# Kernel tuning notes

Hardware: AMD Instinct MI355X
Metric: run time of the kernel (lower is better)

The kernel has to match this reference:

```python
import jax, jax.numpy as jnp
import numpy as np

B, L, H, NH, HD, IT = 16, 512, 256, 8, 32, 2
NEG = -9e15


def _ln(x, g, b):
    m = x.mean(-1, keepdims=True)
    v = ((x - m) ** 2).mean(-1, keepdims=True)
    return (x - m) / jnp.sqrt(v + 1e-5) * g + b


def setup_inputs() -> dict:
    key = jax.random.key(0)
    ks = jax.random.split(key, 12)

    def nrm(k, shape, fan_in):
        return jax.random.normal(k, shape, dtype=jnp.float32) / np.float32(np.sqrt(fan_in))

    return {
        "data": jax.random.normal(ks[0], (B, L, H), jnp.float32),
        "gat_WQ_w": nrm(ks[1], (NH, H, H), H),
        "gat_WQ_b": jnp.zeros((NH, H), jnp.float32),
        "gat_a1": nrm(ks[2], (NH, 3 * H), 3 * H),
        "gat_a2": nrm(ks[3], (NH, 3 * H), 3 * H),
        "gat_fc_w": nrm(ks[4], (NH, 3 * H, HD), 3 * H),
        "gat_fc_b": jnp.zeros((NH, HD), jnp.float32),
        "norm_g": jnp.ones((IT, H), jnp.float32),
        "norm_b": jnp.zeros((IT, H), jnp.float32),
        "sq_w": nrm(ks[5], (IT, NH * HD, H), H),
        "sq_b": jnp.zeros((IT, NH * HD), jnp.float32),
        "sk_w": nrm(ks[6], (IT, NH * HD, H), H),
        "sk_b": jnp.zeros((IT, NH * HD), jnp.float32),
        "so_w": nrm(ks[7], (IT, H, NH * HD), NH * HD),
        "so_b": jnp.zeros((IT, H), jnp.float32),
        "fc_w": nrm(ks[8], (NH * HD, H), NH * HD),
        "fc_b": jnp.zeros((H,), jnp.float32),
        "mask": jax.random.randint(ks[9], (B, L), 0, 2, jnp.int32),
        "edge_matrix": jax.random.randint(ks[10], (B, L, L), 0, 2, jnp.int32),
    }


def _gat_head(xn, ax, adj_pos, Wq, bq, a1, a2, Fw, Fb):
    # xn: [B,L,H] normalized nodes; ax: [B,L,2H] interleaved (r_embs, relay)
    h = jnp.concatenate([xn @ Wq.T + bq, ax], axis=-1)  # [B,L,3H]
    # decomposed a^T [h_i ; h_j] = a1.h_i + a2.h_j  (avoids O(N^2*6H) concat)
    ei = h @ a1  # [B,L]
    ej = h @ a2  # [B,L]
    e = jax.nn.leaky_relu(ei[:, :, None] + ej[:, None, :], 0.2)  # [B,L,L]
    att = jax.nn.softmax(jnp.where(adj_pos, e, NEG), axis=2)
    hp = jnp.einsum('bij,bjd->bid', att, h)  # [B,L,3H]
    return jax.nn.elu(hp @ Fw + Fb)  # [B,L,HD]


def _forward(data, gat_WQ_w, gat_WQ_b, gat_a1, gat_a2, gat_fc_w, gat_fc_b,
             norm_g, norm_b, sq_w, sq_b, sk_w, sk_b, so_w, so_b, fc_w, fc_b,
             mask, edge_matrix):
    pad = mask == 0                                   # True at padding positions
    smask = jnp.concatenate([jnp.zeros((B, 1), bool), pad], axis=1)  # [B,L+1]
    adj_pos = edge_matrix > 0
    nodes = data                                      # [B,L,H]
    relay = data.mean(axis=1)                         # [B,H]
    gat = jax.vmap(_gat_head, in_axes=(None, None, None, 0, 0, 0, 0, 0, 0))
    scale = np.float32(1.0 / np.sqrt(HD))

    for i in range(IT):
        xn = _ln(nodes, norm_g[i], norm_b[i])
        # torch views [B,H,2,L] as [B,2H,L]: features interleave (r_embs, relay)
        ax = jnp.stack([data, jnp.broadcast_to(relay[:, None, :], (B, L, H))],
                       axis=-1).reshape(B, L, 2 * H)
        heads = gat(xn, ax, adj_pos, gat_WQ_w, gat_WQ_b, gat_a1, gat_a2,
                    gat_fc_w, gat_fc_b)               # [NH,B,L,HD]
        temp = jnp.transpose(heads, (1, 2, 0, 3)).reshape(B, L, NH * HD)
        nodes = nodes + jax.nn.leaky_relu(temp @ fc_w + fc_b, 0.01)
        # star attention (MSA2); note original uses v = k (WV unused)
        y = jnp.concatenate([relay[:, None, :], nodes], axis=1)   # [B,L+1,H]
        q = (relay @ sq_w[i].T + sq_b[i]).reshape(B, NH, HD)
        k = (y @ sk_w[i].T + sk_b[i]).transpose(0, 2, 1).reshape(B, NH, HD, L + 1)
        v = jnp.swapaxes(k, 2, 3)                                  # [B,NH,L+1,HD]
        pre = jnp.einsum('bnd,bndl->bnl', q, k) * scale
        pre = jnp.where(smask[:, None, :], -jnp.inf, pre)
        al = jax.nn.softmax(pre, axis=2)
        att = jnp.einsum('bnl,bnld->bnd', al, v).reshape(B, NH * HD)
        relay = jax.nn.leaky_relu(att @ so_w[i].T + so_b[i], 0.01)
        nodes = jnp.where(pad[:, :, None], 0.0, nodes)
    return nodes, relay


def reference(data, gat_WQ_w, gat_WQ_b, gat_a1, gat_a2, gat_fc_w, gat_fc_b,
              norm_g, norm_b, sq_w, sq_b, sk_w, sk_b, so_w, so_b, fc_w, fc_b,
              mask, edge_matrix):
    return _forward(data, gat_WQ_w, gat_WQ_b, gat_a1, gat_a2, gat_fc_w, gat_fc_b,
                    norm_g, norm_b, sq_w, sq_b, sk_w, sk_b, so_w, so_b, fc_w, fc_b,
                    mask, edge_matrix)
```

## Files before the change

### kernel.cpp

```cpp
#include <hip/hip_runtime.h>
#include <hip/hip_bf16.h>
#include <math.h>

#define BB 16
#define LL 512
#define HH 256
#define NHEAD 8
#define HDIM 32
#define LP1 513
#define NODES_ELEMS (BB*LL*HH)

typedef __attribute__((ext_vector_type(8))) short bf16x8;
typedef __attribute__((ext_vector_type(4))) float f32x4;

__device__ __forceinline__ unsigned short f2bf(float f) {
  union { float f; unsigned u; } x; x.f = f;
  unsigned r = x.u + 0x7fffu + ((x.u >> 16) & 1u);
  return (unsigned short)(r >> 16);
}
__device__ __forceinline__ float bf2f(unsigned short u) {
  union { unsigned u; float f; } x; x.u = (unsigned)u << 16; return x.f;
}

__global__ __launch_bounds__(256) void mega_prep_kernel(
    const float* __restrict__ data, const int* __restrict__ edge,
    const float* __restrict__ fc_w, const float* __restrict__ fcw,
    const float* __restrict__ sk_w, const float* __restrict__ sq_w,
    const float* __restrict__ so_w, const float* __restrict__ WQw,
    const float* __restrict__ WQb, const float* __restrict__ a1,
    const float* __restrict__ a2,
    unsigned short* __restrict__ datab, unsigned char* __restrict__ ep,
    unsigned short* __restrict__ fcwT, unsigned short* __restrict__ Bcat,
    unsigned short* __restrict__ skwb, float* __restrict__ sqT,
    float* __restrict__ soT, float* __restrict__ rpart,
    float* __restrict__ w1, float* __restrict__ w2,
    float* __restrict__ c1, float* __restrict__ c2,
    float* __restrict__ bqf, float* __restrict__ a1o, float* __restrict__ a2o) {
  __shared__ float smem[64 * 65];
  int blk = blockIdx.x, t = threadIdx.x;
  if (blk < 128) {
    int b = blk >> 3, ch = blk & 7;
    const float* pr = data + ((size_t)b * 512 + ch * 64) * 256 + t;
    unsigned short* db = datab + ((size_t)b * 512 + ch * 64) * 256 + t;
    float s = 0.f;
    for (int l = 0; l < 64; l++) {
      float v = pr[(size_t)l * 256];
      db[(size_t)l * 256] = f2bf(v);
      s += v;
    }
    rpart[(size_t)blk * 256 + t] = s;
  } else if (blk < 2176) {
    int row = (blk - 128) * 4 + (t >> 6);
    int lane = t & 63;
    const int* adj = edge + ((size_t)row << 9);
    unsigned v = 0;
#pragma unroll
    for (int u = 0; u < 8; u++) v |= (adj[lane + 64 * u] > 0 ? 1u : 0u) << u;
    ep[((size_t)row << 6) + lane] = (unsigned char)v;
  } else if (blk < 2432) {
    int idx = (blk - 2176) * 256 + t;
    int d = idx & 31;
    int g = idx >> 5;
    int n = g >> 8, c = g & 255;
    Bcat[((size_t)n * 32 + d) * 512 + 256 + c] =
        f2bf(fcw[((size_t)n * 768 + 256 + 2 * c) * 32 + d]);
  } else if (blk < 2944) {
    int idx = (blk - 2432) * 256 + t;
    skwb[idx] = f2bf(sk_w[idx]);
  } else if (blk < 3024) {
    int q = blk - 2944;
    int mat = q >> 4, tl = q & 15;
    int r0 = (tl >> 2) * 64, c0 = (tl & 3) * 64;
    const float* in;
    if (mat == 0) in = fc_w;
    else if (mat <= 2) in = sq_w + (mat - 1) * 65536;
    else in = so_w + (mat - 3) * 65536;
    int cc = t & 63, rq = t >> 6;
#pragma unroll
    for (int i = 0; i < 16; i++) {
      int r = rq + i * 4;
      smem[r * 65 + cc] = in[(r0 + r) * 256 + c0 + cc];
    }
    __syncthreads();
#pragma unroll
    for (int i = 0; i < 16; i++) {
      int cp = rq + i * 4;
      float v = smem[cc * 65 + cp];
      if (mat == 0) fcwT[(c0 + cp) * 256 + r0 + cc] = f2bf(v);
      else if (mat <= 2) sqT[(mat - 1) * 65536 + (c0 + cp) * 256 + r0 + cc] = v;
      else soT[(mat - 3) * 65536 + (c0 + cp) * 256 + r0 + cc] = v;
    }
  } else if (blk < 3152) {
    int q = blk - 3024;
    int n = q >> 4, kc = q & 15;
    int k = kc * 16 + (t & 15), cseg = t >> 4;
    float s1 = 0.f, s2 = 0.f;
#pragma unroll
    for (int u = 0; u < 16; u++) {
      int c = cseg * 16 + u;
      float wv = WQw[((size_t)(n * 256 + c)) * 256 + k];
      s1 = fmaf(a1[n * 768 + c], wv, s1);
      s2 = fmaf(a2[n * 768 + c], wv, s2);
    }
    smem[cseg * 16 + (t & 15)] = s1;
    smem[256 + cseg * 16 + (t & 15)] = s2;
    __syncthreads();
    if (cseg == 0) {
      float a = 0.f, b2 = 0.f;
#pragma unroll
      for (int u = 0; u < 16; u++) {
        a += smem[u * 16 + (t & 15)];
        b2 += smem[256 + u * 16 + (t & 15)];
      }
      w1[n * 256 + k] = a;
      w2[n * 256 + k] = b2;
    }
  } else if (blk < 3160) {
    int n = blk - 3152;
    int d = t & 31, seg = t >> 5;
    float s = 0.f;
#pragma unroll
    for (int u = 0; u < 32; u++) {
      int c = seg * 32 + u;
      s = fmaf(WQb[n * 256 + c], fcw[((size_t)n * 768 + c) * 32 + d], s);
    }
    smem[seg * 32 + d] = s;
    __syncthreads();
    if (seg == 0) {
      float a = 0.f;
#pragma unroll
      for (int u = 0; u < 8; u++) a += smem[u * 32 + d];
      bqf[n * 32 + d] = a;
    }
  } else if (blk == 3160) {
    int n = t >> 5, sl = t & 31;
    float s1 = 0.f, s2 = 0.f;
#pragma unroll
    for (int u = 0; u < 8; u++) {
      int c = sl * 8 + u;
      float wb = WQb[n * 256 + c];
      s1 = fmaf(a1[n * 768 + c], wb, s1);
      s2 = fmaf(a2[n * 768 + c], wb, s2);
    }
    smem[t] = s1; smem[256 + t] = s2;
    __syncthreads();
    if (sl == 0) {
      float a = 0.f, b2 = 0.f;
      for (int u = 0; u < 32; u++) { a += smem[n * 32 + u]; b2 += smem[256 + n * 32 + u]; }
      c1[n] = a; c2[n] = b2;
    }
  } else {
#pragma unroll
    for (int n = 0; n < 8; n++) {
      a1o[n * 256 + t] = a1[n * 768 + 256 + 2 * t];
      a2o[n * 256 + t] = a2[n * 768 + 256 + 2 * t];
    }
  }
}

__device__ __forceinline__ void rarf_tail(
    int n, int b, int t, const float* rel,
    const float* __restrict__ a1, const float* __restrict__ a2,
    const float* __restrict__ fcw, const float* __restrict__ fcb,
    const float* __restrict__ bqf,
    float* __restrict__ ra1, float* __restrict__ ra2, float* __restrict__ rf,
    float* red1, float* red2, float* pf_s) {
  int lane = t & 63, w = t >> 6;
  float p1 = rel[t] * a1[n * 768 + 257 + 2 * t];
  float p2 = rel[t] * a2[n * 768 + 257 + 2 * t];
#pragma unroll
  for (int o = 32; o; o >>= 1) { p1 += __shfl_xor(p1, o); p2 += __shfl_xor(p2, o); }
  if (lane == 0) { red1[w] = p1; red2[w] = p2; }
  int d = t & 31, seg = t >> 5;
  float pf = 0.f;
  for (int u = 0; u < 32; u++) {
    int k = seg * 32 + u;
    pf = fmaf(rel[k], fcw[((size_t)n * 768 + 257 + 2 * k) * 32 + d], pf);
  }
  pf_s[seg * 33 + d] = pf;
  __syncthreads();
  if (t == 0) {
    ra1[n * 16 + b] = red1[0] + red1[1] + red1[2] + red1[3];
    ra2[n * 16 + b] = red2[0] + red2[1] + red2[2] + red2[3];
  }
  if (t < 32) {
    float s = 0.f;
    for (int gg = 0; gg < 8; gg++) s += pf_s[gg * 33 + t];
    rf[((size_t)n * 16 + b) * 32 + t] = s + fcb[n * 32 + t] + bqf[n * 32 + t];
  }
}

__global__ __launch_bounds__(256) void prep2_kernel(
    const float* __restrict__ WQw, const float* __restrict__ fcw,
    unsigned short* __restrict__ Bcat,
    const float* __restrict__ rpart,
    const unsigned short* __restrict__ skw0, const float* __restrict__ skb0,
    const float* __restrict__ a1, const float* __restrict__ a2,
    const float* __restrict__ fcb, const float* __restrict__ bqf,
    float* __restrict__ relay, unsigned short* __restrict__ ktb,
    float* __restrict__ ra1, float* __restrict__ ra2, float* __restrict__ rf) {
  __shared__ float smem[12288];
  int blk = blockIdx.x, t = threadIdx.x;
  if (blk < 128) {
    float* wq_s = smem;
    float* fw_s = smem + 4096;
    int n = blk >> 4, kt = blk & 15;
#pragma unroll
    for (int i = 0; i < 16; i++) {
      int c = i * 16 + (t >> 4), kk = t & 15;
      wq_s[c * 16 + kk] = WQw[(size_t)n * 65536 + c * 256 + kt * 16 + kk];
    }
#pragma unroll
    for (int i = 0; i < 32; i++) {
      int idx = i * 256 + t;
      fw_s[(idx >> 5) * 32 + (idx & 31)] = fcw[(size_t)n * 24576 + idx];
    }
    __syncthreads();
    int kloc = t >> 4, dp = t & 15;
    float a0 = 0.f, a1v = 0.f;
    for (int c = 0; c < 256; c++) {
      float wv = wq_s[c * 16 + kloc];
      a0 = fmaf(wv, fw_s[c * 32 + dp * 2], a0);
      a1v = fmaf(wv, fw_s[c * 32 + dp * 2 + 1], a1v);
    }
    int k = kt * 16 + kloc;
    Bcat[((size_t)n * 32 + dp * 2) * 512 + k] = f2bf(a0);
    Bcat[((size_t)n * 32 + dp * 2 + 1) * 512 + k] = f2bf(a1v);
  } else {
    float* rel = smem;
    float* red1 = smem + 256;
    float* red2 = smem + 264;
    float* pf_s = smem + 272;
    int id = blk - 128;
    int n = id >> 4, b = id & 15;
    float s = 0.f;
#pragma unroll
    for (int ch = 0; ch < 8; ch++) s += rpart[((size_t)(b * 8 + ch)) * 256 + t];
    s *= (1.0f / 512.0f);
    rel[t] = s;
    __syncthreads();
    if (n == 0) {
      relay[b * 256 + t] = s;
      float acc = 0.f;
      for (int k = 0; k < 256; k++) acc = fmaf(rel[k], bf2f(skw0[(size_t)t * 256 + k]), acc);
      ktb[((size_t)b * LP1) * 256 + t] = f2bf(acc + skb0[t]);
    }
    rarf_tail(n, b, t, rel, a1, a2, fcw, fcb, bqf, ra1, ra2, rf, red1, red2, pf_s);
  }
}

__global__ __launch_bounds__(256) void so_rarf_kernel(
    const float* __restrict__ atts,
    const float* __restrict__ soT_it, const float* __restrict__ sob_it,
    const unsigned short* __restrict__ skw_nx, const float* __restrict__ skb_nx,
    const float* __restrict__ a1, const float* __restrict__ a2,
    const float* __restrict__ fcw, const float* __restrict__ fcb,
    const float* __restrict__ bqf, int do_extras,
    float* __restrict__ relay, unsigned short* __restrict__ ktb,
    float* __restrict__ ra1, float* __restrict__ ra2, float* __restrict__ rf) {
  int n = blockIdx.x >> 4, b = blockIdx.x & 15;
  if (!do_extras && n > 0) return;
  __shared__ float xr[256];
  __shared__ float rel[256];
  __shared__ float red1[4], red2[4];
  __shared__ float pf_s[8 * 33];
  int t = threadIdx.x;
  xr[t] = atts[b * 256 + t];
  __syncthreads();
  float acc = 0.f;
  for (int k = 0; k < 256; k++) acc = fmaf(xr[k], soT_it[(size_t)k * 256 + t], acc);
  float v = acc + sob_it[t];
  v = v > 0.f ? v : 0.01f * v;
  rel[t] = v;
  __syncthreads();
  if (n == 0) relay[b * 256 + t] = v;
  if (!do_extras) return;
  if (n == 0) {
    float a2v = 0.f;
    for (int k = 0; k < 256; k++) a2v = fmaf(rel[k], bf2f(skw_nx[(size_t)t * 256 + k]), a2v);
    ktb[((size_t)b * LP1) * 256 + t] = f2bf(a2v + skb_nx[t]);
  }
  rarf_tail(n, b, t, rel, a1, a2, fcw, fcb, bqf, ra1, ra2, rf, red1, red2, pf_s);
}

__global__ __launch_bounds__(256) void lnei_kernel(const float* __restrict__ src,
                                                   const unsigned short* __restrict__ datab,
                                                   const float* __restrict__ g,
                                                   const float* __restrict__ bb,
                                                   const float* __restrict__ w1,
                                                   const float* __restrict__ w2,
                                                   const float* __restrict__ a1o,
                                                   const float* __restrict__ a2o,
                                                   const float* __restrict__ c1,
                                                   const float* __restrict__ c2,
                                                   const float* __restrict__ ra1,
                                                   const float* __restrict__ ra2,
                                                   unsigned short* __restrict__ xnb,
                                                   float* __restrict__ ei,
                                                   float* __restrict__ ej) {
  int r = blockIdx.x * 4 + (threadIdx.x >> 6);
  int b = r >> 9;
  int lane = threadIdx.x & 63;
  float x[4], dv[4];
#pragma unroll
  for (int u = 0; u < 4; u++) {
    int c = lane + 64 * u;
    x[u] = src[(size_t)r * 256 + c];
    dv[u] = bf2f(datab[(size_t)r * 256 + c]);
  }
  float s = x[0] + x[1] + x[2] + x[3];
#pragma unroll
  for (int o = 32; o; o >>= 1) s += __shfl_xor(s, o);
  float mean = s * (1.0f / 256.0f);
  float v = 0.f;
#pragma unroll
  for (int u = 0; u < 4; u++) { x[u] -= mean; v = fmaf(x[u], x[u], v); }
#pragma unroll
  for (int o = 32; o; o >>= 1) v += __shfl_xor(v, o);
  float rstd = rsqrtf(v * (1.0f / 256.0f) + 1e-5f);
  float xv[4];
#pragma unroll
  for (int u = 0; u < 4; u++) {
    int c = lane + 64 * u;
    xv[u] = x[u] * rstd * g[c] + bb[c];
    xnb[(size_t)r * 256 + c] = f2bf(xv[u]);
  }
  float s1a[8], s2a[8];
#pragma unroll
  for (int n = 0; n < 8; n++) {
    float s1 = 0.f, s2 = 0.f;
#pragma unroll
    for (int u = 0; u < 4; u++) {
      int c = lane + 64 * u;
      s1 = fmaf(xv[u], w1[n * 256 + c], s1);
      s1 = fmaf(dv[u], a1o[n * 256 + c], s1);
      s2 = fmaf(xv[u], w2[n * 256 + c], s2);
      s2 = fmaf(dv[u], a2o[n * 256 + c], s2);
    }
    s1a[n] = s1; s2a[n] = s2;
  }
#pragma unroll
  for (int o = 32; o; o >>= 1) {
#pragma unroll
    for (int n = 0; n < 8; n++) {
      s1a[n] += __shfl_xor(s1a[n], o);
      s2a[n] += __shfl_xor(s2a[n], o);
    }
  }
  if (lane == 0) {
#pragma unroll
    for (int n = 0; n < 8; n++) {
      ei[n * 8192 + r] = s1a[n] + c1[n] + ra1[n * 16 + b];
      ej[n * 8192 + r] = s2a[n] + c2[n] + ra2[n * 16 + b];
    }
  }
}

__global__ __launch_bounds__(256) void g_gemm_kernel(
    const unsigned short* __restrict__ A1, const unsigned short* __restrict__ A2,
    const unsigned short* __restrict__ Bcat, unsigned short* __restrict__ GT) {
  int tileN = blockIdx.x * 64;
  int tileM = blockIdx.y * 128;
  int t = threadIdx.x;
  int wv = t >> 6, lane = t & 63;
  int lo = lane & 15, quad = lane >> 4;
  int rowBase0 = tileM + wv * 32;
  const unsigned short* ap1[2];
  const unsigned short* ap2[2];
#pragma unroll
  for (int rt = 0; rt < 2; rt++) {
    int arow = rowBase0 + rt * 16 + lo;
    ap1[rt] = A1 + (size_t)arow * 256 + quad * 8;
    ap2[rt] = A2 + (size_t)arow * 256 + quad * 8;
  }
  f32x4 acc[2][4] = {};
  for (int k0 = 0; k0 < 512; k0 += 32) {
    bf16x8 af[2];
#pragma unroll
    for (int rt = 0; rt < 2; rt++)
      af[rt] = (k0 < 256) ? *(const bf16x8*)(ap1[rt] + k0)
                          : *(const bf16x8*)(ap2[rt] + k0 - 256);
#pragma unroll
    for (int ct = 0; ct < 4; ct++) {
      bf16x8 bf_ = *(const bf16x8*)(Bcat + (size_t)(tileN + ct * 16 + lo) * 512 + k0 + quad * 8);
#pragma unroll
      for (int rt = 0; rt < 2; rt++)
        acc[rt][ct] = __builtin_amdgcn_mfma_f32_16x16x32_bf16(af[rt], bf_, acc[rt][ct], 0, 0, 0);
    }
  }
#pragma unroll
  for (int rt = 0; rt < 2; rt++) {
#pragma unroll
    for (int ct = 0; ct < 4; ct++) {
      int co = tileN + ct * 16 + lo;
      int n = co >> 5, d = co & 31;
      int jrow = rowBase0 + rt * 16 + quad * 4;
      int b2 = jrow >> 9, jj = jrow & 511;
      ushort4 pk;
      pk.x = f2bf(acc[rt][ct][0]);
      pk.y = f2bf(acc[rt][ct][1]);
      pk.z = f2bf(acc[rt][ct][2]);
      pk.w = f2bf(acc[rt][ct][3]);
      *(ushort4*)&GT[(((size_t)(n * 16 + b2) * 32 + d) << 9) + jj] = pk;
    }
  }
}

__global__ __launch_bounds__(256) void gat_agg_kernel(
    const unsigned short* __restrict__ GT,
    const float* __restrict__ ei, const float* __restrict__ ej,
    const unsigned char* __restrict__ ep,
    const float* __restrict__ rf,
    unsigned short* __restrict__ tempb) {
  __shared__ unsigned short W[32][512];
  __shared__ float denom_s[32];
  int blk = blockIdx.x;
  int sib = blk >> 7;
  int g = blk & 127;
  int n = g >> 4;
  int b = g & 15;
  int i0 = sib << 5;
  int t = threadIdx.x;
  int wv = t >> 6, lane = t & 63;
  int lo = lane & 15, quad = lane >> 4;

  const float* ejrow = ej + n * 8192 + b * 512;
  float ejv[8];
#pragma unroll
  for (int u = 0; u < 8; u++) ejv[u] = ejrow[lane + 64 * u];
  float mm = ejv[0];
#pragma unroll
  for (int u = 1; u < 8; u++) mm = fmaxf(mm, ejv[u]);
#pragma unroll
  for (int o = 32; o; o >>= 1) mm = fmaxf(mm, __shfl_xor(mm, o));

  for (int rr = 0; rr < 8; rr++) {
    int row = wv * 8 + rr;
    float eiv = ei[n * 8192 + b * 512 + i0 + row];
    float M = eiv + mm;
    M = M > 0.f ? M : 0.2f * M;
    unsigned pb = ep[(((size_t)(b * 512 + i0 + row)) << 6) + lane];
    int rx = (row & 7) << 3;
#pragma unroll
    for (int u = 0; u < 8; u++) {
      float e = eiv + ejv[u];
      e = e > 0.f ? e : 0.2f * e;
      float w = ((pb >> u) & 1) ? __expf(e - M) : 0.f;
      int col = lane + 64 * u;
      W[row][((col >> 3 << 3) ^ rx) + (col & 7)] = f2bf(w);
    }
  }
  __syncthreads();

  int rt = wv >> 1, dh = wv & 1;
  int arow = rt * 16 + lo;
  int rx = arow & 7;
  const unsigned short* gtb = GT + (((size_t)(n * 16 + b) * 32) << 9);
  bf16x8 bones;
  {
    short ov = (lo == 0) ? (short)0x3F80 : (short)0;
#pragma unroll
    for (int j = 0; j < 8; j++) bones[j] = ov;
  }
  f32x4 acc = {}, accd = {};
  for (int k0 = 0; k0 < 512; k0 += 32) {
    int chunk = (k0 >> 3) + quad;
    bf16x8 a0 = *(const bf16x8*)&W[arow][(chunk ^ rx) << 3];
    bf16x8 bf_ = *(const bf16x8*)(gtb + (((size_t)(dh * 16 + lo)) << 9) + k0 + quad * 8);
    acc = __builtin_amdgcn_mfma_f32_16x16x32_bf16(a0, bf_, acc, 0, 0, 0);
    if (dh == 0)
      accd = __builtin_amdgcn_mfma_f32_16x16x32_bf16(a0, bones, accd, 0, 0, 0);
  }
  if (dh == 0 && lo == 0) {
#pragma unroll
    for (int r = 0; r < 4; r++) denom_s[rt * 16 + quad * 4 + r] = accd[r];
  }
  __syncthreads();
  int d = dh * 16 + lo;
  float base = rf[((size_t)n * 16 + b) * 32 + d];
#pragma unroll
  for (int r = 0; r < 4; r++) {
    int row = rt * 16 + quad * 4 + r;
    float inv = 1.0f / fmaxf(denom_s[row], 1e-35f);
    float v = acc[r] * inv + base;
    v = v > 0.f ? v : expm1f(v);
    tempb[((size_t)(b * 512 + i0 + row)) * 256 + n * 32 + d] = f2bf(v);
  }
}

__global__ __launch_bounds__(256) void fc_kt_kernel(
    const unsigned short* __restrict__ tempb,
    const unsigned short* __restrict__ fcwT,
    const float* __restrict__ fc_b,
    const unsigned short* __restrict__ skw_it,
    const float* __restrict__ skb_it,
    const int* __restrict__ mask,
    const float* __restrict__ resid,
    float* __restrict__ nodes,
    unsigned short* __restrict__ ktb) {
  __shared__ unsigned short tmp[32][264];
  int blk = blockIdx.x;
  int b = blk >> 4;
  int i0 = (blk & 15) << 5;
  int t = threadIdx.x;
  int wv = t >> 6, lane = t & 63;
  int lo = lane & 15, quad = lane >> 4;
  int ch = wv >> 1, rt2 = wv & 1;

  const unsigned short* arow_p = tempb + ((size_t)(b * 512 + i0 + rt2 * 16 + lo)) * 256 + quad * 8;
  f32x4 facc[8] = {};
  for (int k0 = 0; k0 < 256; k0 += 32) {
    bf16x8 a0 = *(const bf16x8*)(arow_p + k0);
#pragma unroll
    for (int ct = 0; ct < 8; ct++) {
      int co = ch * 128 + ct * 16 + lo;
      bf16x8 bf_ = *(const bf16x8*)(fcwT + (size_t)co * 256 + k0 + quad * 8);
      facc[ct] = __builtin_amdgcn_mfma_f32_16x16x32_bf16(a0, bf_, facc[ct], 0, 0, 0);
    }
  }
#pragma unroll
  for (int ct = 0; ct < 8; ct++) {
    int co = ch * 128 + ct * 16 + lo;
    float bv = fc_b[co];
#pragma unroll
    for (int r = 0; r < 4; r++) {
      int row = rt2 * 16 + quad * 4 + r;
      int grow = b * 512 + i0 + row;
      float v = facc[ct][r] + bv;
      v = v > 0.f ? v : 0.01f * v;
      v = (mask[grow] != 0) ? resid[(size_t)grow * 256 + co] + v : 0.f;
      nodes[(size_t)grow * 256 + co] = v;
      tmp[row][co] = f2bf(v);
    }
  }
  __syncthreads();

  f32x4 kacc[8] = {};
  for (int k0 = 0; k0 < 256; k0 += 32) {
    bf16x8 a0 = *(const bf16x8*)&tmp[rt2 * 16 + lo][k0 + quad * 8];
#pragma unroll
    for (int ct = 0; ct < 8; ct++) {
      int co = ch * 128 + ct * 16 + lo;
      bf16x8 bf_ = *(const bf16x8*)(skw_it + (size_t)co * 256 + k0 + quad * 8);
      kacc[ct] = __builtin_amdgcn_mfma_f32_16x16x32_bf16(a0, bf_, kacc[ct], 0, 0, 0);
    }
  }
#pragma unroll
  for (int ct = 0; ct < 8; ct++) {
    int co = ch * 128 + ct * 16 + lo;
    float bv = skb_it[co];
#pragma unroll
    for (int r = 0; r < 4; r++) {
      int row = rt2 * 16 + quad * 4 + r;
      int yrow = b * LP1 + 1 + i0 + row;
      ktb[(size_t)yrow * 256 + co] = f2bf(kacc[ct][r] + bv);
    }
  }
}

__global__ __launch_bounds__(256) void star_attn_kernel(const float* __restrict__ relay,
                                                        const float* __restrict__ sqT_it,
                                                        const float* __restrict__ sqb_it,
                                                        const unsigned short* __restrict__ ktb,
                                                        const int* __restrict__ mask,
                                                        float* __restrict__ attstar) {
  int n = blockIdx.x >> 4, b = blockIdx.x & 15;
  int t = threadIdx.x;
  int lane = t & 63, w = t >> 6;
  __shared__ float relb[256];
  __shared__ float qv[32];
  __shared__ float pre[LP1];
  __shared__ float red[4];
  __shared__ float par[8][33];
  relb[t] = relay[b * 256 + t];
  __syncthreads();
  {
    int d = t & 31, g = t >> 5;
    float qp = 0.f;
    for (int k = 0; k < 32; k++)
      qp = fmaf(relb[g * 32 + k], sqT_it[(size_t)(g * 32 + k) * 256 + n * 32 + d], qp);
    par[g][d] = qp;
  }
  __syncthreads();
  if (t < 32) {
    float q = 0.f;
#pragma unroll
    for (int gg = 0; gg < 8; gg++) q += par[gg][t];
    qv[t] = q + sqb_it[n * 32 + t];
  }
  __syncthreads();
  const float scale = 0.17677669529663687f;
  for (int l = t; l < LP1; l += 256) {
    bool masked = (l > 0) && (mask[b * LL + l - 1] == 0);
    float p;
    if (masked) p = -3.4e38f;
    else {
      p = 0.f;
      const unsigned short* krow = ktb + ((size_t)b * LP1 + l) * 256 + n * 32;
#pragma unroll
      for (int d = 0; d < 32; d++) p = fmaf(qv[d], bf2f(krow[d]), p);
      p *= scale;
    }
    pre[l] = p;
  }
  __syncthreads();
  float m = -3.4e38f;
  for (int l = t; l < LP1; l += 256) m = fmaxf(m, pre[l]);
#pragma unroll
  for (int o = 32; o; o >>= 1) m = fmaxf(m, __shfl_xor(m, o));
  if (lane == 0) red[w] = m;
  __syncthreads();
  m = fmaxf(fmaxf(red[0], red[1]), fmaxf(red[2], red[3]));
  __syncthreads();
  float s = 0.f;
  for (int l = t; l < LP1; l += 256) {
    float wv = __expf(pre[l] - m);
    pre[l] = wv;
    s += wv;
  }
#pragma unroll
  for (int o = 32; o; o >>= 1) s += __shfl_xor(s, o);
  if (lane == 0) red[w] = s;
  __syncthreads();
  float denom = red[0] + red[1] + red[2] + red[3];
  int d = t & 31, g = t >> 5;
  float acc = 0.f;
  for (int l = g; l < LP1; l += 8)
    acc = fmaf(pre[l], bf2f(ktb[((size_t)b * LP1 + l) * 256 + n * 32 + d]), acc);
  par[g][d] = acc;
  __syncthreads();
  if (t < 32) {
    float a = 0.f;
    for (int gg = 0; gg < 8; gg++) a += par[gg][t];
    attstar[b * 256 + n * 32 + t] = a / denom;
  }
}

extern "C" void kernel_launch(void* const* d_in, const int* in_sizes, int n_in,
                              void* d_out, int out_size, void* d_ws, size_t ws_size,
                              hipStream_t stream) {
  const float* data  = (const float*)d_in[0];
  const float* WQw   = (const float*)d_in[1];
  const float* WQb   = (const float*)d_in[2];
  const float* a1    = (const float*)d_in[3];
  const float* a2    = (const float*)d_in[4];
  const float* fcw_g = (const float*)d_in[5];
  const float* fcb_g = (const float*)d_in[6];
  const float* ng    = (const float*)d_in[7];
  const float* nb    = (const float*)d_in[8];
  const float* sq_w  = (const float*)d_in[9];
  const float* sq_b  = (const float*)d_in[10];
  const float* sk_w  = (const float*)d_in[11];
  const float* sk_b  = (const float*)d_in[12];
  const float* so_w  = (const float*)d_in[13];
  const float* so_b  = (const float*)d_in[14];
  const float* fc_w  = (const float*)d_in[15];
  const float* fc_b  = (const float*)d_in[16];
  const int*   mask  = (const int*)d_in[17];
  const int*   edge  = (const int*)d_in[18];

  float* nodes = (float*)d_out;
  float* relay = nodes + NODES_ELEMS;

  char* p = (char*)d_ws;
  auto alloc = [&](size_t bytes) -> char* {
    char* r = p; p += (bytes + 255) & ~(size_t)255; return r;
  };
  unsigned short* xnb  = (unsigned short*)alloc((size_t)8192 * 256 * 2);
  unsigned short* datab= (unsigned short*)alloc((size_t)8192 * 256 * 2);
  unsigned short* GT   = (unsigned short*)alloc((size_t)8 * 16 * 32 * 512 * 2);
  unsigned short* tmpb = (unsigned short*)alloc((size_t)8192 * 256 * 2);
  unsigned short* ktb  = (unsigned short*)alloc((size_t)8208 * 256 * 2);
  unsigned char* ep    = (unsigned char*)alloc((size_t)8192 * 64);
  float* ei            = (float*)alloc(65536 * 4);
  float* ej            = (float*)alloc(65536 * 4);
  float* ra1           = (float*)alloc(128 * 4);
  float* ra2           = (float*)alloc(128 * 4);
  float* rf            = (float*)alloc(4096 * 4);
  float* bqf           = (float*)alloc(256 * 4);
  float* w1            = (float*)alloc(2048 * 4);
  float* w2            = (float*)alloc(2048 * 4);
  float* c1            = (float*)alloc(8 * 4);
  float* c2            = (float*)alloc(8 * 4);
  float* a1o           = (float*)alloc(2048 * 4);
  float* a2o           = (float*)alloc(2048 * 4);
  float* rpart         = (float*)alloc(128 * 256 * 4);
  unsigned short* Bcat = (unsigned short*)alloc((size_t)256 * 512 * 2);
  unsigned short* fcwT = (unsigned short*)alloc((size_t)65536 * 2);
  unsigned short* skwb = (unsigned short*)alloc((size_t)131072 * 2);
  float* sqT           = (float*)alloc((size_t)131072 * 4);
  float* soT           = (float*)alloc((size_t)131072 * 4);
  float* atts          = (float*)alloc(4096 * 4);

  mega_prep_kernel<<<3162, 256, 0, stream>>>(data, edge, fc_w, fcw_g, sk_w, sq_w,
                                             so_w, WQw, WQb, a1, a2,
                                             datab, ep, fcwT, Bcat, skwb, sqT, soT,
                                             rpart, w1, w2, c1, c2, bqf, a1o, a2o);
  prep2_kernel<<<256, 256, 0, stream>>>(WQw, fcw_g, Bcat, rpart, skwb, sk_b,
                                        a1, a2, fcb_g, bqf,
                                        relay, ktb, ra1, ra2, rf);

  for (int it = 0; it < 2; it++) {
    const float* src = (it == 0) ? data : nodes;
    lnei_kernel<<<2048, 256, 0, stream>>>(src, datab, ng + it * 256, nb + it * 256,
                                          w1, w2, a1o, a2o, c1, c2, ra1, ra2,
                                          xnb, ei, ej);
    g_gemm_kernel<<<dim3(4, 64), 256, 0, stream>>>(xnb, datab, Bcat, GT);
    gat_agg_kernel<<<NHEAD * BB * 16, 256, 0, stream>>>(GT, ei, ej, ep, rf, tmpb);
    fc_kt_kernel<<<256, 256, 0, stream>>>(tmpb, fcwT, fc_b,
                                          skwb + it * 65536, sk_b + it * 256,
                                          mask, src, nodes, ktb);
    star_attn_kernel<<<BB * NHEAD, 256, 0, stream>>>(relay, sqT + it * 65536,
                                                     sq_b + it * 256, ktb, mask, atts);
    so_rarf_kernel<<<128, 256, 0, stream>>>(atts, soT + it * 65536, so_b + it * 256,
                                            skwb + 65536, sk_b + 256,
                                            a1, a2, fcw_g, fcb_g, bqf,
                                            (it == 0) ? 1 : 0,
                                            relay, ktb, ra1, ra2, rf);
  }
}
```

Measured before the change: 353.4 us.

## Fuse layernorm and ei/ej projections into the G GEMM kernel

```diff
diff --git a/kernel.cpp b/kernel.cpp
--- a/kernel.cpp
+++ b/kernel.cpp
@@ -197,6 +197,8 @@
     const unsigned short* __restrict__ skw0, const float* __restrict__ skb0,
     const float* __restrict__ a1, const float* __restrict__ a2,
     const float* __restrict__ fcb, const float* __restrict__ bqf,
+    const float* __restrict__ w1, const float* __restrict__ w2,
+    const float* __restrict__ a1o, const float* __restrict__ a2o,
     float* __restrict__ relay, unsigned short* __restrict__ ktb,
     float* __restrict__ ra1, float* __restrict__ ra2, float* __restrict__ rf) {
   __shared__ float smem[12288];
@@ -226,7 +228,7 @@
     int k = kt * 16 + kloc;
     Bcat[((size_t)n * 32 + dp * 2) * 512 + k] = f2bf(a0);
     Bcat[((size_t)n * 32 + dp * 2 + 1) * 512 + k] = f2bf(a1v);
-  } else {
+  } else if (blk < 256) {
     float* rel = smem;
     float* red1 = smem + 256;
     float* red2 = smem + 264;
@@ -246,6 +248,17 @@
       ktb[((size_t)b * LP1) * 256 + t] = f2bf(acc + skb0[t]);
     }
     rarf_tail(n, b, t, rel, a1, a2, fcw, fcb, bqf, ra1, ra2, rf, red1, red2, pf_s);
+  } else {
+    int q = blk - 256;
+    int n = q & 7, isEj = q >> 3;
+    const float* wsrc = isEj ? w2 : w1;
+    const float* asrc = isEj ? a2o : a1o;
+#pragma unroll
+    for (int h = 0; h < 2; h++) {
+      int k = h * 256 + t;
+      float v = (k < 256) ? wsrc[n * 256 + k] : asrc[n * 256 + k - 256];
+      Bcat[((size_t)(256 + q)) * 512 + k] = f2bf(v);
+    }
   }
 }
 
@@ -283,125 +296,108 @@
   rarf_tail(n, b, t, rel, a1, a2, fcw, fcb, bqf, ra1, ra2, rf, red1, red2, pf_s);
 }
 
-__global__ __launch_bounds__(256) void lnei_kernel(const float* __restrict__ src,
-                                                   const unsigned short* __restrict__ datab,
-                                                   const float* __restrict__ g,
-                                                   const float* __restrict__ bb,
-                                                   const float* __restrict__ w1,
-                                                   const float* __restrict__ w2,
-                                                   const float* __restrict__ a1o,
-                                                   const float* __restrict__ a2o,
-                                                   const float* __restrict__ c1,
-                                                   const float* __restrict__ c2,
-                                                   const float* __restrict__ ra1,
-                                                   const float* __restrict__ ra2,
-                                                   unsigned short* __restrict__ xnb,
-                                                   float* __restrict__ ei,
-                                                   float* __restrict__ ej) {
-  int r = blockIdx.x * 4 + (threadIdx.x >> 6);
-  int b = r >> 9;
-  int lane = threadIdx.x & 63;
-  float x[4], dv[4];
-#pragma unroll
-  for (int u = 0; u < 4; u++) {
-    int c = lane + 64 * u;
-    x[u] = src[(size_t)r * 256 + c];
-    dv[u] = bf2f(datab[(size_t)r * 256 + c]);
-  }
-  float s = x[0] + x[1] + x[2] + x[3];
-#pragma unroll
-  for (int o = 32; o; o >>= 1) s += __shfl_xor(s, o);
-  float mean = s * (1.0f / 256.0f);
-  float v = 0.f;
-#pragma unroll
-  for (int u = 0; u < 4; u++) { x[u] -= mean; v = fmaf(x[u], x[u], v); }
-#pragma unroll
-  for (int o = 32; o; o >>= 1) v += __shfl_xor(v, o);
-  float rstd = rsqrtf(v * (1.0f / 256.0f) + 1e-5f);
-  float xv[4];
-#pragma unroll
-  for (int u = 0; u < 4; u++) {
-    int c = lane + 64 * u;
-    xv[u] = x[u] * rstd * g[c] + bb[c];
-    xnb[(size_t)r * 256 + c] = f2bf(xv[u]);
-  }
-  float s1a[8], s2a[8];
-#pragma unroll
-  for (int n = 0; n < 8; n++) {
-    float s1 = 0.f, s2 = 0.f;
-#pragma unroll
-    for (int u = 0; u < 4; u++) {
-      int c = lane + 64 * u;
-      s1 = fmaf(xv[u], w1[n * 256 + c], s1);
-      s1 = fmaf(dv[u], a1o[n * 256 + c], s1);
-      s2 = fmaf(xv[u], w2[n * 256 + c], s2);
-      s2 = fmaf(dv[u], a2o[n * 256 + c], s2);
-    }
-    s1a[n] = s1; s2a[n] = s2;
-  }
-#pragma unroll
-  for (int o = 32; o; o >>= 1) {
-#pragma unroll
-    for (int n = 0; n < 8; n++) {
-      s1a[n] += __shfl_xor(s1a[n], o);
-      s2a[n] += __shfl_xor(s2a[n], o);
-    }
-  }
-  if (lane == 0) {
-#pragma unroll
-    for (int n = 0; n < 8; n++) {
-      ei[n * 8192 + r] = s1a[n] + c1[n] + ra1[n * 16 + b];
-      ej[n * 8192 + r] = s2a[n] + c2[n] + ra2[n * 16 + b];
-    }
-  }
-}
-
-__global__ __launch_bounds__(256) void g_gemm_kernel(
-    const unsigned short* __restrict__ A1, const unsigned short* __restrict__ A2,
-    const unsigned short* __restrict__ Bcat, unsigned short* __restrict__ GT) {
-  int tileN = blockIdx.x * 64;
-  int tileM = blockIdx.y * 128;
+__global__ __launch_bounds__(256) void lng_gemm_kernel(
+    const float* __restrict__ src,
+    const unsigned short* __restrict__ datab,
+    const unsigned short* __restrict__ Bcat,
+    const float* __restrict__ g, const float* __restrict__ bb,
+    const float* __restrict__ c1, const float* __restrict__ c2,
+    const float* __restrict__ ra1, const float* __restrict__ ra2,
+    unsigned short* __restrict__ GT,
+    float* __restrict__ ei, float* __restrict__ ej) {
+  __shared__ unsigned short A[32][520];
+  int blk = blockIdx.x;
+  int b = blk >> 4;
+  int i0 = (blk & 15) << 5;
   int t = threadIdx.x;
   int wv = t >> 6, lane = t & 63;
   int lo = lane & 15, quad = lane >> 4;
-  int rowBase0 = tileM + wv * 32;
-  const unsigned short* ap1[2];
-  const unsigned short* ap2[2];
-#pragma unroll
-  for (int rt = 0; rt < 2; rt++) {
-    int arow = rowBase0 + rt * 16 + lo;
-    ap1[rt] = A1 + (size_t)arow * 256 + quad * 8;
-    ap2[rt] = A2 + (size_t)arow * 256 + quad * 8;
-  }
+
+  float4 g4 = *(const float4*)(g + lane * 4);
+  float4 b4 = *(const float4*)(bb + lane * 4);
+  float xs[8][4];
+  float sum[8], sq[8];
+#pragma unroll
+  for (int rr = 0; rr < 8; rr++) {
+    int grow = b * 512 + i0 + wv * 8 + rr;
+    float4 v = *(const float4*)(src + (size_t)grow * 256 + lane * 4);
+    xs[rr][0] = v.x; xs[rr][1] = v.y; xs[rr][2] = v.z; xs[rr][3] = v.w;
+    sum[rr] = v.x + v.y + v.z + v.w;
+    sq[rr] = v.x * v.x + v.y * v.y + v.z * v.z + v.w * v.w;
+    ushort4 dv4 = *(const ushort4*)(datab + (size_t)grow * 256 + lane * 4);
+    *(ushort4*)&A[wv * 8 + rr][256 + lane * 4] = dv4;
+  }
+#pragma unroll
+  for (int o = 32; o; o >>= 1) {
+#pragma unroll
+    for (int rr = 0; rr < 8; rr++) {
+      sum[rr] += __shfl_xor(sum[rr], o);
+      sq[rr] += __shfl_xor(sq[rr], o);
+    }
+  }
+#pragma unroll
+  for (int rr = 0; rr < 8; rr++) {
+    float mean = sum[rr] * (1.0f / 256.0f);
+    float var = sq[rr] * (1.0f / 256.0f) - mean * mean;
+    float rstd = rsqrtf(var + 1e-5f);
+    ushort4 pk;
+    pk.x = f2bf((xs[rr][0] - mean) * rstd * g4.x + b4.x);
+    pk.y = f2bf((xs[rr][1] - mean) * rstd * g4.y + b4.y);
+    pk.z = f2bf((xs[rr][2] - mean) * rstd * g4.z + b4.z);
+    pk.w = f2bf((xs[rr][3] - mean) * rstd * g4.w + b4.w);
+    *(ushort4*)&A[wv * 8 + rr][lane * 4] = pk;
+  }
+  __syncthreads();
+
   f32x4 acc[2][4] = {};
+  f32x4 acce[2] = {};
   for (int k0 = 0; k0 < 512; k0 += 32) {
     bf16x8 af[2];
 #pragma unroll
     for (int rt = 0; rt < 2; rt++)
-      af[rt] = (k0 < 256) ? *(const bf16x8*)(ap1[rt] + k0)
-                          : *(const bf16x8*)(ap2[rt] + k0 - 256);
-#pragma unroll
-    for (int ct = 0; ct < 4; ct++) {
-      bf16x8 bf_ = *(const bf16x8*)(Bcat + (size_t)(tileN + ct * 16 + lo) * 512 + k0 + quad * 8);
+      af[rt] = *(const bf16x8*)&A[rt * 16 + lo][k0 + quad * 8];
+#pragma unroll
+    for (int j = 0; j < 4; j++) {
+      int tile = j * 4 + wv;
+      bf16x8 bf_ = *(const bf16x8*)(Bcat + (size_t)(tile * 16 + lo) * 512 + k0 + quad * 8);
 #pragma unroll
       for (int rt = 0; rt < 2; rt++)
-        acc[rt][ct] = __builtin_amdgcn_mfma_f32_16x16x32_bf16(af[rt], bf_, acc[rt][ct], 0, 0, 0);
-    }
-  }
-#pragma unroll
-  for (int rt = 0; rt < 2; rt++) {
-#pragma unroll
-    for (int ct = 0; ct < 4; ct++) {
-      int co = tileN + ct * 16 + lo;
-      int n = co >> 5, d = co & 31;
-      int jrow = rowBase0 + rt * 16 + quad * 4;
-      int b2 = jrow >> 9, jj = jrow & 511;
+        acc[rt][j] = __builtin_amdgcn_mfma_f32_16x16x32_bf16(af[rt], bf_, acc[rt][j], 0, 0, 0);
+    }
+    if (wv == 0) {
+      bf16x8 bf_ = *(const bf16x8*)(Bcat + (size_t)(256 + lo) * 512 + k0 + quad * 8);
+#pragma unroll
+      for (int rt = 0; rt < 2; rt++)
+        acce[rt] = __builtin_amdgcn_mfma_f32_16x16x32_bf16(af[rt], bf_, acce[rt], 0, 0, 0);
+    }
+  }
+#pragma unroll
+  for (int j = 0; j < 4; j++) {
+    int tile = j * 4 + wv;
+    int co = tile * 16 + lo;
+    int n = co >> 5, d = co & 31;
+#pragma unroll
+    for (int rt = 0; rt < 2; rt++) {
+      int jj = i0 + rt * 16 + quad * 4;
       ushort4 pk;
-      pk.x = f2bf(acc[rt][ct][0]);
-      pk.y = f2bf(acc[rt][ct][1]);
-      pk.z = f2bf(acc[rt][ct][2]);
-      pk.w = f2bf(acc[rt][ct][3]);
-      *(ushort4*)&GT[(((size_t)(n * 16 + b2) * 32 + d) << 9) + jj] = pk;
+      pk.x = f2bf(acc[rt][j][0]);
+      pk.y = f2bf(acc[rt][j][1]);
+      pk.z = f2bf(acc[rt][j][2]);
+      pk.w = f2bf(acc[rt][j][3]);
+      *(ushort4*)&GT[(((size_t)(n * 16 + b) * 32 + d) << 9) + jj] = pk;
+    }
+  }
+  if (wv == 0) {
+    int n = lo & 7, isEj = lo >> 3;
+    float cst = isEj ? (c2[n] + ra2[n * 16 + b]) : (c1[n] + ra1[n * 16 + b]);
+    float* outp = isEj ? ej : ei;
+#pragma unroll
+    for (int rt = 0; rt < 2; rt++) {
+#pragma unroll
+      for (int r = 0; r < 4; r++) {
+        int row = i0 + rt * 16 + quad * 4 + r;
+        outp[n * 8192 + b * 512 + row] = acce[rt][r] + cst;
+      }
     }
   }
 }
@@ -666,7 +662,6 @@
   auto alloc = [&](size_t bytes) -> char* {
     char* r = p; p += (bytes + 255) & ~(size_t)255; return r;
   };
-  unsigned short* xnb  = (unsigned short*)alloc((size_t)8192 * 256 * 2);
   unsigned short* datab= (unsigned short*)alloc((size_t)8192 * 256 * 2);
   unsigned short* GT   = (unsigned short*)alloc((size_t)8 * 16 * 32 * 512 * 2);
   unsigned short* tmpb = (unsigned short*)alloc((size_t)8192 * 256 * 2);
@@ -685,7 +680,7 @@
   float* a1o           = (float*)alloc(2048 * 4);
   float* a2o           = (float*)alloc(2048 * 4);
   float* rpart         = (float*)alloc(128 * 256 * 4);
-  unsigned short* Bcat = (unsigned short*)alloc((size_t)256 * 512 * 2);
+  unsigned short* Bcat = (unsigned short*)alloc((size_t)288 * 512 * 2);
   unsigned short* fcwT = (unsigned short*)alloc((size_t)65536 * 2);
   unsigned short* skwb = (unsigned short*)alloc((size_t)131072 * 2);
   float* sqT           = (float*)alloc((size_t)131072 * 4);
@@ -696,16 +691,15 @@
                                              so_w, WQw, WQb, a1, a2,
                                              datab, ep, fcwT, Bcat, skwb, sqT, soT,
                                              rpart, w1, w2, c1, c2, bqf, a1o, a2o);
-  prep2_kernel<<<256, 256, 0, stream>>>(WQw, fcw_g, Bcat, rpart, skwb, sk_b,
-                                        a1, a2, fcb_g, bqf,
+  prep2_kernel<<<272, 256, 0, stream>>>(WQw, fcw_g, Bcat, rpart, skwb, sk_b,
+                                        a1, a2, fcb_g, bqf, w1, w2, a1o, a2o,
                                         relay, ktb, ra1, ra2, rf);
 
   for (int it = 0; it < 2; it++) {
     const float* src = (it == 0) ? data : nodes;
-    lnei_kernel<<<2048, 256, 0, stream>>>(src, datab, ng + it * 256, nb + it * 256,
-                                          w1, w2, a1o, a2o, c1, c2, ra1, ra2,
-                                          xnb, ei, ej);
-    g_gemm_kernel<<<dim3(4, 64), 256, 0, stream>>>(xnb, datab, Bcat, GT);
+    lng_gemm_kernel<<<256, 256, 0, stream>>>(src, datab, Bcat,
+                                             ng + it * 256, nb + it * 256,
+                                             c1, c2, ra1, ra2, GT, ei, ej);
     gat_agg_kernel<<<NHEAD * BB * 16, 256, 0, stream>>>(GT, ei, ej, ep, rf, tmpb);
     fc_kt_kernel<<<256, 256, 0, stream>>>(tmpb, fcwT, fc_b,
                                           skwb + it * 65536, sk_b + it * 256,
```

Measured after the change: 328.3 us. 1.08x faster.
